# Performance work log

Hardware: AMD Instinct MI355X
Metric: run time of the kernel (lower is better)

## Reference

```python
import jax, jax.numpy as jnp
import numpy as np

B, IN, H, L, S = 256, 256, 256, 2, 128


def setup_inputs() -> dict:
    key = jax.random.key(0)
    ks = jax.random.split(key, 13)
    inp = {
        "x": jax.random.normal(ks[0], (B, IN), jnp.float32),
        "hidden_stack": jax.random.normal(ks[1], (S + 1, B, H, L), jnp.float32) * 0.1,
        "cell_stack": jax.random.normal(ks[2], (S + 1, B, H, L), jnp.float32) * 0.1,
        "w_ih0": jax.random.normal(ks[3], (4 * H, IN), jnp.float32) / np.sqrt(IN).astype(np.float32),
        "w_hh0": jax.random.normal(ks[4], (4 * H, H), jnp.float32) / np.sqrt(H).astype(np.float32),
        "b_ih0": jax.random.normal(ks[5], (4 * H,), jnp.float32) * 0.01,
        "b_hh0": jax.random.normal(ks[6], (4 * H,), jnp.float32) * 0.01,
        "w_ih1": jax.random.normal(ks[7], (4 * H, H), jnp.float32) / np.sqrt(H).astype(np.float32),
        "w_hh1": jax.random.normal(ks[8], (4 * H, H), jnp.float32) / np.sqrt(H).astype(np.float32),
        "b_ih1": jax.random.normal(ks[9], (4 * H,), jnp.float32) * 0.01,
        "b_hh1": jax.random.normal(ks[10], (4 * H,), jnp.float32) * 0.01,
        "op": jax.random.randint(ks[11], (B,), 0, 3, jnp.int32) - 1,  # {-1,0,1}: pop/hold/push
        "pos": jax.random.randint(ks[12], (B,), 1, S, jnp.int32),      # in-bounds for pos+1 and pos+op
    }
    return inp


def _lstm_cell(x, h, c, w_ih, w_hh, b_ih, b_hh):
    # torch.nn.LSTMCell gate order: input, forget, cell(g), output
    g = x @ w_ih.T + h @ w_hh.T + b_ih + b_hh  # (B, 4H)
    i, f, gg, o = jnp.split(g, 4, axis=-1)
    c2 = jax.nn.sigmoid(f) * c + jax.nn.sigmoid(i) * jnp.tanh(gg)
    h2 = jax.nn.sigmoid(o) * jnp.tanh(c2)
    return h2, c2


def reference(x, hidden_stack, cell_stack, w_ih0, w_hh0, b_ih0, b_hh0,
              w_ih1, w_hh1, b_ih1, b_hh1, op, pos):
    bidx = jnp.arange(x.shape[0])
    # gather current top-of-stack state: (B, H, L)
    cur_h = hidden_stack[pos, bidx]
    cur_c = cell_stack[pos, bidx]
    # two-layer LSTM cell (layer 1 feeds on layer 0 hidden)
    h0, c0 = _lstm_cell(x, cur_h[..., 0], cur_c[..., 0], w_ih0, w_hh0, b_ih0, b_hh0)
    h1, c1 = _lstm_cell(h0, cur_h[..., 1], cur_c[..., 1], w_ih1, w_hh1, b_ih1, b_hh1)
    next_h = jnp.stack([h0, h1], axis=-1)  # (B, H, L)
    next_c = jnp.stack([c0, c1], axis=-1)
    # scatter new state at pos+1
    hidden_stack = hidden_stack.at[pos + 1, bidx].set(next_h)
    cell_stack = cell_stack.at[pos + 1, bidx].set(next_c)
    # move stack pointer, gather return state
    new_pos = pos + op
    ret_h = hidden_stack[new_pos, bidx]  # (B, H, L)
    ret_c = cell_stack[new_pos, bidx]
    # faithful to torch source: hidden_ret[:, :, -1] -> shape (1, B, L)
    h_out = ret_h[:, -1, :][None]
    c_out = ret_c[:, -1, :][None]
    return h_out, c_out, hidden_stack, cell_stack
```

## Files before the change

### kernel.cpp

```cpp
#include <hip/hip_runtime.h>


static __device__ __forceinline__ float sigf(float x) {
    return 1.0f / (1.0f + __expf(-x));
}
static __device__ __forceinline__ float tanh_fast(float x) {
    return 2.0f / (1.0f + __expf(-2.0f * x)) - 1.0f;
}

#define GBM 16
#define GBN 64
#define GBK 32

#define NV4_PER_STACK 4227072
#define STACK_ELEMS   16908288
#define CEL_CHUNK1    655360

static __device__ __forceinline__ void copy_span(
    int cb0, const float4* __restrict__ csrc, float4* __restrict__ cdst, int cn4)
{
    int stride = (gridDim.x - cb0) * 256;
    for (int i = (blockIdx.x - cb0) * 256 + threadIdx.x; i < cn4; i += stride)
        cdst[i] = csrc[i];
}

__global__ __launch_bounds__(256) void gemm_copy_k(
    const float* __restrict__ a_lo,
    const float* __restrict__ a_hi,
    const int*   __restrict__ pos,
    const float* __restrict__ wih,
    const float* __restrict__ whh,
    const float* __restrict__ bih,
    const float* __restrict__ bhh,
    float* __restrict__ gates,
    const float4* __restrict__ csrc,
    float4* __restrict__ cdst,
    int cn4)
{
    if (blockIdx.x >= 256) {
        copy_span(256, csrc, cdst, cn4);
        return;
    }
    __shared__ float As[GBK][GBM + 1];
    __shared__ float Ws[GBK][GBN + 4];
    int t   = threadIdx.x;
    int bm0 = (blockIdx.x >> 4) * GBM;
    int jt0 = (blockIdx.x & 15) * GBN;
    int arow = t >> 4;
    int akk  = (t & 15) * 2;
    int wrow = t >> 2;
    int wkb  = (t & 3) * 8;
    int tx = t & 15, ty = t >> 4;
    int ab = bm0 + arow;
    int ap = pos[ab];
    int wj = jt0 + wrow;

    float2 apre;
    float4 wpre0, wpre1;
    {
        int k = akk;
        apre = *(const float2*)&a_lo[ab * 256 + k];
        const float* ws = &wih[wj * 256 + wkb];
        wpre0 = *(const float4*)ws;
        wpre1 = *(const float4*)(ws + 4);
    }
    float acc[4] = {0.f, 0.f, 0.f, 0.f};
    for (int kt = 0; kt < 512; kt += GBK) {
        __syncthreads();
        As[akk][arow]     = apre.x;
        As[akk + 1][arow] = apre.y;
        Ws[wkb][wrow]     = wpre0.x;
        Ws[wkb + 1][wrow] = wpre0.y;
        Ws[wkb + 2][wrow] = wpre0.z;
        Ws[wkb + 3][wrow] = wpre0.w;
        Ws[wkb + 4][wrow] = wpre1.x;
        Ws[wkb + 5][wrow] = wpre1.y;
        Ws[wkb + 6][wrow] = wpre1.z;
        Ws[wkb + 7][wrow] = wpre1.w;
        int kt2 = kt + GBK;
        if (kt2 < 512) {
            int k = kt2 + akk;
            if (k < 256) {
                apre = *(const float2*)&a_lo[ab * 256 + k];
            } else {
                const float* ah = a_hi + ((ap * 256 + ab) * 256 + (k - 256)) * 2;
                apre.x = ah[0];
                apre.y = ah[2];
            }
            int kk = kt2 + wkb;
            const float* ws = (kk < 256) ? &wih[wj * 256 + kk]
                                         : &whh[wj * 256 + kk - 256];
            wpre0 = *(const float4*)ws;
            wpre1 = *(const float4*)(ws + 4);
        }
        __syncthreads();
        #pragma unroll
        for (int k = 0; k < GBK; ++k) {
            float a   = As[k][ty];
            float4 bv = *(const float4*)&Ws[k][tx * 4];
            acc[0] = fmaf(a, bv.x, acc[0]);
            acc[1] = fmaf(a, bv.y, acc[1]);
            acc[2] = fmaf(a, bv.z, acc[2]);
            acc[3] = fmaf(a, bv.w, acc[3]);
        }
    }
    int j = jt0 + tx * 4;
    float4 b0 = *(const float4*)&bih[j];
    float4 b1 = *(const float4*)&bhh[j];
    float4 r;
    r.x = acc[0] + b0.x + b1.x;
    r.y = acc[1] + b0.y + b1.y;
    r.z = acc[2] + b0.z + b1.z;
    r.w = acc[3] + b0.w + b1.w;
    *(float4*)&gates[(bm0 + ty) * 1024 + j] = r;
}

__global__ __launch_bounds__(256) void act0_copy_k(
    const float* __restrict__ gates,
    const float* __restrict__ cel,
    const int*   __restrict__ pos,
    float* __restrict__ h0f, float* __restrict__ c0f,
    const float4* __restrict__ csrc,
    float4* __restrict__ cdst,
    int cn4)
{
    if (blockIdx.x >= 256) {
        copy_span(256, csrc, cdst, cn4);
        return;
    }
    int e = blockIdx.x * 256 + threadIdx.x;
    int b = e >> 8, h = e & 255;
    float cin = cel[((pos[b] * 256 + b) * 256 + h) * 2];
    const float* g = gates + b * 1024 + h;
    float gi = g[0], gf = g[256], gg = g[512], go = g[768];
    float c  = sigf(gf) * cin + sigf(gi) * tanh_fast(gg);
    h0f[e] = sigf(go) * tanh_fast(c);
    c0f[e] = c;
}

static __device__ __forceinline__ void lstm1(
    const float* __restrict__ gates, const float* __restrict__ cel,
    int p, int b, int h, float& hv, float& cv)
{
    float cin = cel[((p * 256 + b) * 256 + h) * 2 + 1];
    const float* g = gates + b * 1024 + h;
    float gi = g[0], gf = g[256], gg = g[512], go = g[768];
    cv = sigf(gf) * cin + sigf(gi) * tanh_fast(gg);
    hv = sigf(go) * tanh_fast(cv);
}

__global__ __launch_bounds__(256) void slot_k(
    const float* __restrict__ hid, const float* __restrict__ cel,
    const int* __restrict__ pos, const int* __restrict__ op,
    const float* __restrict__ h0f, const float* __restrict__ c0f,
    const float* __restrict__ gates,
    float* __restrict__ out)
{
    if (blockIdx.x == 256) {
        int b = threadIdx.x;
        int o = op[b];
        int p = pos[b];
        float h0v, h1v, c0v, c1v;
        if (o == 1) {
            h0v = h0f[b * 256 + 255];
            c0v = c0f[b * 256 + 255];
            lstm1(gates, cel, p, b, 255, h1v, c1v);
        } else {
            int base2 = (((p + o) * 256 + b) * 256 + 255) * 2;
            h0v = hid[base2]; h1v = hid[base2 + 1];
            c0v = cel[base2]; c1v = cel[base2 + 1];
        }
        out[b * 2]           = h0v;
        out[b * 2 + 1]       = h1v;
        out[512 + b * 2]     = c0v;
        out[512 + b * 2 + 1] = c1v;
        return;
    }
    int v = blockIdx.x * 256 + threadIdx.x;
    bool is_cell = v >= 32768;
    int vv = v & 32767;
    int b = vv >> 7;
    int q = vv & 127;
    int p = pos[b];
    int h = q * 2;
    float h1a, c1a, h1b, c1b;
    lstm1(gates, cel, p, b, h,     h1a, c1a);
    lstm1(gates, cel, p, b, h + 1, h1b, c1b);
    float4 val;
    if (is_cell) {
        val.x = c0f[b * 256 + h];     val.y = c1a;
        val.z = c0f[b * 256 + h + 1]; val.w = c1b;
    } else {
        val.x = h0f[b * 256 + h];     val.y = h1a;
        val.z = h0f[b * 256 + h + 1]; val.w = h1b;
    }
    float4* dst = (float4*)(out + 1024 + (is_cell ? STACK_ELEMS : 0));
    dst[(p + 1) * 32768 + b * 128 + q] = val;
}

extern "C" void kernel_launch(void* const* d_in, const int* in_sizes, int n_in,
                              void* d_out, int out_size, void* d_ws, size_t ws_size,
                              hipStream_t stream) {
    const float* x    = (const float*)d_in[0];
    const float* hid  = (const float*)d_in[1];
    const float* cel  = (const float*)d_in[2];
    const float* wih0 = (const float*)d_in[3];
    const float* whh0 = (const float*)d_in[4];
    const float* bih0 = (const float*)d_in[5];
    const float* bhh0 = (const float*)d_in[6];
    const float* wih1 = (const float*)d_in[7];
    const float* whh1 = (const float*)d_in[8];
    const float* bih1 = (const float*)d_in[9];
    const float* bhh1 = (const float*)d_in[10];
    const int* op  = (const int*)d_in[11];
    const int* pos = (const int*)d_in[12];
    float* out = (float*)d_out;

    float* W     = (float*)d_ws;
    float* gates = W;
    float* h0f   = W + 262144;
    float* c0f   = W + 327680;

    float4*       hid_out = (float4*)(out + 1024);
    float4*       cel_out = (float4*)(out + 1024 + STACK_ELEMS);
    const float4* hid_in  = (const float4*)hid;
    const float4* cel_in  = (const float4*)cel;

    gemm_copy_k<<<256 + 2048, 256, 0, stream>>>(
        x, hid, pos, wih0, whh0, bih0, bhh0, gates,
        hid_in, hid_out, NV4_PER_STACK);
    act0_copy_k<<<256 + 1024, 256, 0, stream>>>(
        gates, cel, pos, h0f, c0f,
        cel_in, cel_out, CEL_CHUNK1);
    gemm_copy_k<<<256 + 2048, 256, 0, stream>>>(
        h0f, hid + 1, pos, wih1, whh1, bih1, bhh1, gates,
        cel_in + CEL_CHUNK1, cel_out + CEL_CHUNK1,
        NV4_PER_STACK - CEL_CHUNK1);
    slot_k<<<257, 256, 0, stream>>>(
        hid, cel, pos, op, h0f, c0f, gates, out);
}
```

Before: 266.7 us.

## Split-K GEMM with larger register tiles and rebalanced stack-copy overlap

The gate GEMM switches to a 32x128 block tile with a 4x4 register tile per thread, and splits K across up to four blocks. Each split writes partial sums to workspace, and the activation kernels add those partials plus the biases. The bulk stack copies are redistributed across the three overlapped launches: a first hidden chunk, then the hidden remainder plus the first cell chunk, then the rest of the cell stack. The aim is more FMA work per shared-memory load and a better balance of the copy traffic against each compute phase, at the cost of extra partial-sum traffic and reduction reads.

```diff
diff --git a/kernel.cpp b/kernel.cpp
--- a/kernel.cpp
+++ b/kernel.cpp
@@ -8,20 +8,26 @@
     return 2.0f / (1.0f + __expf(-2.0f * x)) - 1.0f;
 }
 
-#define GBM 16
-#define GBN 64
-#define GBK 32
-
 #define NV4_PER_STACK 4227072
 #define STACK_ELEMS   16908288
-#define CEL_CHUNK1    655360
-
-static __device__ __forceinline__ void copy_span(
-    int cb0, const float4* __restrict__ csrc, float4* __restrict__ cdst, int cn4)
-{
-    int stride = (gridDim.x - cb0) * 256;
-    for (int i = (blockIdx.x - cb0) * 256 + threadIdx.x; i < cn4; i += stride)
-        cdst[i] = csrc[i];
+
+static __device__ __forceinline__ void copy_spans(
+    int cb0, int nb1,
+    const float4* __restrict__ s1, float4* __restrict__ d1, int n1,
+    const float4* __restrict__ s2, float4* __restrict__ d2, int n2)
+{
+    int cb = blockIdx.x - cb0;
+    int ncopy = gridDim.x - cb0;
+    if (cb < nb1) {
+        int stride = nb1 * 256;
+        for (int i = cb * 256 + threadIdx.x; i < n1; i += stride)
+            d1[i] = s1[i];
+    } else if (n2 > 0) {
+        int nb2 = ncopy - nb1;
+        int stride = nb2 * 256;
+        for (int i = (cb - nb1) * 256 + threadIdx.x; i < n2; i += stride)
+            d2[i] = s2[i];
+    }
 }
 
 __global__ __launch_bounds__(256) void gemm_copy_k(
@@ -30,121 +36,147 @@
     const int*   __restrict__ pos,
     const float* __restrict__ wih,
     const float* __restrict__ whh,
-    const float* __restrict__ bih,
-    const float* __restrict__ bhh,
-    float* __restrict__ gates,
-    const float4* __restrict__ csrc,
-    float4* __restrict__ cdst,
-    int cn4)
-{
-    if (blockIdx.x >= 256) {
-        copy_span(256, csrc, cdst, cn4);
+    float* __restrict__ gpart, int nks,
+    int nb1, const float4* __restrict__ cs1, float4* __restrict__ cd1, int cn1,
+    const float4* __restrict__ cs2, float4* __restrict__ cd2, int cn2)
+{
+    int ncomp = nks << 6;
+    if ((int)blockIdx.x >= ncomp) {
+        copy_spans(ncomp, nb1, cs1, cd1, cn1, cs2, cd2, cn2);
         return;
     }
-    __shared__ float As[GBK][GBM + 1];
-    __shared__ float Ws[GBK][GBN + 4];
+
+    __shared__ float As[32][36];
+    __shared__ float Ws[32][132];
+
     int t   = threadIdx.x;
-    int bm0 = (blockIdx.x >> 4) * GBM;
-    int jt0 = (blockIdx.x & 15) * GBN;
-    int arow = t >> 4;
-    int akk  = (t & 15) * 2;
-    int wrow = t >> 2;
-    int wkb  = (t & 3) * 8;
-    int tx = t & 15, ty = t >> 4;
-    int ab = bm0 + arow;
-    int ap = pos[ab];
-    int wj = jt0 + wrow;
-
-    float2 apre;
-    float4 wpre0, wpre1;
-    {
-        int k = akk;
-        apre = *(const float2*)&a_lo[ab * 256 + k];
-        const float* ws = &wih[wj * 256 + wkb];
-        wpre0 = *(const float4*)ws;
-        wpre1 = *(const float4*)(ws + 4);
-    }
-    float acc[4] = {0.f, 0.f, 0.f, 0.f};
-    for (int kt = 0; kt < 512; kt += GBK) {
-        __syncthreads();
-        As[akk][arow]     = apre.x;
-        As[akk + 1][arow] = apre.y;
-        Ws[wkb][wrow]     = wpre0.x;
-        Ws[wkb + 1][wrow] = wpre0.y;
-        Ws[wkb + 2][wrow] = wpre0.z;
-        Ws[wkb + 3][wrow] = wpre0.w;
-        Ws[wkb + 4][wrow] = wpre1.x;
-        Ws[wkb + 5][wrow] = wpre1.y;
-        Ws[wkb + 6][wrow] = wpre1.z;
-        Ws[wkb + 7][wrow] = wpre1.w;
-        int kt2 = kt + GBK;
-        if (kt2 < 512) {
-            int k = kt2 + akk;
-            if (k < 256) {
-                apre = *(const float2*)&a_lo[ab * 256 + k];
+    int ks  = blockIdx.x >> 6;
+    int tb  = blockIdx.x & 63;
+    int bm0 = (tb >> 3) << 5;
+    int jt0 = (tb & 7) << 7;
+    int kspan = 512 / nks;
+    int k0  = ks * kspan;
+    int nsub = kspan >> 5;
+
+    int arow = t >> 3;
+    int ak4  = (t & 7) << 2;
+    int ab   = bm0 + arow;
+    int ap   = pos[ab];
+    int wrow = t >> 1;
+    int wk   = (t & 1) << 4;
+    int wj   = jt0 + wrow;
+    int tx = t & 31, ty = t >> 5;
+
+    float acc[4][4] = {{0.f}};
+    for (int s = 0; s < nsub; ++s) {
+        int kb = k0 + (s << 5);
+        {
+            int kg = kb + ak4;
+            if (kg < 256) {
+                float4 v = *(const float4*)&a_lo[ab * 256 + kg];
+                As[ak4 + 0][arow] = v.x;
+                As[ak4 + 1][arow] = v.y;
+                As[ak4 + 2][arow] = v.z;
+                As[ak4 + 3][arow] = v.w;
             } else {
-                const float* ah = a_hi + ((ap * 256 + ab) * 256 + (k - 256)) * 2;
-                apre.x = ah[0];
-                apre.y = ah[2];
+                const float* ah = a_hi + ((ap * 256 + ab) * 256 + (kg - 256)) * 2;
+                As[ak4 + 0][arow] = ah[0];
+                As[ak4 + 1][arow] = ah[2];
+                As[ak4 + 2][arow] = ah[4];
+                As[ak4 + 3][arow] = ah[6];
             }
-            int kk = kt2 + wkb;
-            const float* ws = (kk < 256) ? &wih[wj * 256 + kk]
-                                         : &whh[wj * 256 + kk - 256];
-            wpre0 = *(const float4*)ws;
-            wpre1 = *(const float4*)(ws + 4);
+        }
+        {
+            int kg = kb + wk;
+            const float* ws = (kg < 256) ? &wih[wj * 256 + kg]
+                                         : &whh[wj * 256 + kg - 256];
+            #pragma unroll
+            for (int i = 0; i < 4; ++i) {
+                float4 v = *(const float4*)(ws + i * 4);
+                Ws[wk + i * 4 + 0][wrow] = v.x;
+                Ws[wk + i * 4 + 1][wrow] = v.y;
+                Ws[wk + i * 4 + 2][wrow] = v.z;
+                Ws[wk + i * 4 + 3][wrow] = v.w;
+            }
         }
         __syncthreads();
         #pragma unroll
-        for (int k = 0; k < GBK; ++k) {
-            float a   = As[k][ty];
-            float4 bv = *(const float4*)&Ws[k][tx * 4];
-            acc[0] = fmaf(a, bv.x, acc[0]);
-            acc[1] = fmaf(a, bv.y, acc[1]);
-            acc[2] = fmaf(a, bv.z, acc[2]);
-            acc[3] = fmaf(a, bv.w, acc[3]);
-        }
-    }
-    int j = jt0 + tx * 4;
-    float4 b0 = *(const float4*)&bih[j];
-    float4 b1 = *(const float4*)&bhh[j];
-    float4 r;
-    r.x = acc[0] + b0.x + b1.x;
-    r.y = acc[1] + b0.y + b1.y;
-    r.z = acc[2] + b0.z + b1.z;
-    r.w = acc[3] + b0.w + b1.w;
-    *(float4*)&gates[(bm0 + ty) * 1024 + j] = r;
+        for (int k = 0; k < 32; ++k) {
+            float4 av = *(const float4*)&As[k][ty << 2];
+            float4 wv = *(const float4*)&Ws[k][tx << 2];
+            float w0 = wv.x, w1 = wv.y, w2 = wv.z, w3 = wv.w;
+            acc[0][0] = fmaf(av.x, w0, acc[0][0]);
+            acc[0][1] = fmaf(av.x, w1, acc[0][1]);
+            acc[0][2] = fmaf(av.x, w2, acc[0][2]);
+            acc[0][3] = fmaf(av.x, w3, acc[0][3]);
+            acc[1][0] = fmaf(av.y, w0, acc[1][0]);
+            acc[1][1] = fmaf(av.y, w1, acc[1][1]);
+            acc[1][2] = fmaf(av.y, w2, acc[1][2]);
+            acc[1][3] = fmaf(av.y, w3, acc[1][3]);
+            acc[2][0] = fmaf(av.z, w0, acc[2][0]);
+            acc[2][1] = fmaf(av.z, w1, acc[2][1]);
+            acc[2][2] = fmaf(av.z, w2, acc[2][2]);
+            acc[2][3] = fmaf(av.z, w3, acc[2][3]);
+            acc[3][0] = fmaf(av.w, w0, acc[3][0]);
+            acc[3][1] = fmaf(av.w, w1, acc[3][1]);
+            acc[3][2] = fmaf(av.w, w2, acc[3][2]);
+            acc[3][3] = fmaf(av.w, w3, acc[3][3]);
+        }
+        __syncthreads();
+    }
+    float* gp = gpart + ks * 262144 + (bm0 + (ty << 2)) * 1024 + jt0 + (tx << 2);
+    #pragma unroll
+    for (int i = 0; i < 4; ++i) {
+        float4 r;
+        r.x = acc[i][0]; r.y = acc[i][1]; r.z = acc[i][2]; r.w = acc[i][3];
+        *(float4*)&gp[i * 1024] = r;
+    }
 }
 
 __global__ __launch_bounds__(256) void act0_copy_k(
-    const float* __restrict__ gates,
+    const float* __restrict__ gpart, int nks,
     const float* __restrict__ cel,
     const int*   __restrict__ pos,
+    const float* __restrict__ bih, const float* __restrict__ bhh,
     float* __restrict__ h0f, float* __restrict__ c0f,
-    const float4* __restrict__ csrc,
-    float4* __restrict__ cdst,
-    int cn4)
+    int nb1, const float4* __restrict__ cs1, float4* __restrict__ cd1, int cn1,
+    const float4* __restrict__ cs2, float4* __restrict__ cd2, int cn2)
 {
     if (blockIdx.x >= 256) {
-        copy_span(256, csrc, cdst, cn4);
+        copy_spans(256, nb1, cs1, cd1, cn1, cs2, cd2, cn2);
         return;
     }
     int e = blockIdx.x * 256 + threadIdx.x;
     int b = e >> 8, h = e & 255;
+    float gi = bih[h]       + bhh[h];
+    float gf = bih[256 + h] + bhh[256 + h];
+    float gg = bih[512 + h] + bhh[512 + h];
+    float go = bih[768 + h] + bhh[768 + h];
+    const float* gp = gpart + b * 1024 + h;
+    for (int ks = 0; ks < nks; ++ks, gp += 262144) {
+        gi += gp[0]; gf += gp[256]; gg += gp[512]; go += gp[768];
+    }
     float cin = cel[((pos[b] * 256 + b) * 256 + h) * 2];
-    const float* g = gates + b * 1024 + h;
-    float gi = g[0], gf = g[256], gg = g[512], go = g[768];
     float c  = sigf(gf) * cin + sigf(gi) * tanh_fast(gg);
     h0f[e] = sigf(go) * tanh_fast(c);
     c0f[e] = c;
 }
 
-static __device__ __forceinline__ void lstm1(
-    const float* __restrict__ gates, const float* __restrict__ cel,
+static __device__ __forceinline__ void lstm1p(
+    const float* __restrict__ gpart, int nks,
+    const float* __restrict__ bih, const float* __restrict__ bhh,
+    const float* __restrict__ cel,
     int p, int b, int h, float& hv, float& cv)
 {
+    float gi = bih[h]       + bhh[h];
+    float gf = bih[256 + h] + bhh[256 + h];
+    float gg = bih[512 + h] + bhh[512 + h];
+    float go = bih[768 + h] + bhh[768 + h];
+    const float* gp = gpart + b * 1024 + h;
+    for (int ks = 0; ks < nks; ++ks, gp += 262144) {
+        gi += gp[0]; gf += gp[256]; gg += gp[512]; go += gp[768];
+    }
     float cin = cel[((p * 256 + b) * 256 + h) * 2 + 1];
-    const float* g = gates + b * 1024 + h;
-    float gi = g[0], gf = g[256], gg = g[512], go = g[768];
     cv = sigf(gf) * cin + sigf(gi) * tanh_fast(gg);
     hv = sigf(go) * tanh_fast(cv);
 }
@@ -153,7 +185,8 @@
     const float* __restrict__ hid, const float* __restrict__ cel,
     const int* __restrict__ pos, const int* __restrict__ op,
     const float* __restrict__ h0f, const float* __restrict__ c0f,
-    const float* __restrict__ gates,
+    const float* __restrict__ gpart, int nks,
+    const float* __restrict__ bih, const float* __restrict__ bhh,
     float* __restrict__ out)
 {
     if (blockIdx.x == 256) {
@@ -164,7 +197,7 @@
         if (o == 1) {
             h0v = h0f[b * 256 + 255];
             c0v = c0f[b * 256 + 255];
-            lstm1(gates, cel, p, b, 255, h1v, c1v);
+            lstm1p(gpart, nks, bih, bhh, cel, p, b, 255, h1v, c1v);
         } else {
             int base2 = (((p + o) * 256 + b) * 256 + 255) * 2;
             h0v = hid[base2]; h1v = hid[base2 + 1];
@@ -184,8 +217,8 @@
     int p = pos[b];
     int h = q * 2;
     float h1a, c1a, h1b, c1b;
-    lstm1(gates, cel, p, b, h,     h1a, c1a);
-    lstm1(gates, cel, p, b, h + 1, h1b, c1b);
+    lstm1p(gpart, nks, bih, bhh, cel, p, b, h,     h1a, c1a);
+    lstm1p(gpart, nks, bih, bhh, cel, p, b, h + 1, h1b, c1b);
     float4 val;
     if (is_cell) {
         val.x = c0f[b * 256 + h];     val.y = c1a;
@@ -216,26 +249,36 @@
     const int* pos = (const int*)d_in[12];
     float* out = (float*)d_out;
 
-    float* W     = (float*)d_ws;
-    float* gates = W;
-    float* h0f   = W + 262144;
-    float* c0f   = W + 327680;
-
+    size_t need4 = (size_t)(4 * 262144 + 2 * 65536) * 4;
+    size_t need2 = (size_t)(2 * 262144 + 2 * 65536) * 4;
+    int KS = (ws_size >= need4) ? 4 : (ws_size >= need2 ? 2 : 1);
+    float* gpart = (float*)d_ws;
+    float* h0f   = gpart + (size_t)KS * 262144;
+    float* c0f   = h0f + 65536;
+
+    const float4* hid_in  = (const float4*)hid;
+    const float4* cel_in  = (const float4*)cel;
     float4*       hid_out = (float4*)(out + 1024);
     float4*       cel_out = (float4*)(out + 1024 + STACK_ELEMS);
-    const float4* hid_in  = (const float4*)hid;
-    const float4* cel_in  = (const float4*)cel;
-
-    gemm_copy_k<<<256 + 2048, 256, 0, stream>>>(
-        x, hid, pos, wih0, whh0, bih0, bhh0, gates,
-        hid_in, hid_out, NV4_PER_STACK);
-    act0_copy_k<<<256 + 1024, 256, 0, stream>>>(
-        gates, cel, pos, h0f, c0f,
-        cel_in, cel_out, CEL_CHUNK1);
-    gemm_copy_k<<<256 + 2048, 256, 0, stream>>>(
-        h0f, hid + 1, pos, wih1, whh1, bih1, bhh1, gates,
-        cel_in + CEL_CHUNK1, cel_out + CEL_CHUNK1,
-        NV4_PER_STACK - CEL_CHUNK1);
+
+    const int H1 = 2800000;
+    const int C2 = 1372928;
+    const int NCOPY = 2048;
+    int n2a = NV4_PER_STACK - H1;
+    int nb1_2 = (int)((long long)NCOPY * n2a / (n2a + C2));
+
+    gemm_copy_k<<<64 * KS + NCOPY, 256, 0, stream>>>(
+        x, hid, pos, wih0, whh0, gpart, KS,
+        NCOPY, hid_in, hid_out, H1,
+        (const float4*)0, (float4*)0, 0);
+    act0_copy_k<<<256 + NCOPY, 256, 0, stream>>>(
+        gpart, KS, cel, pos, bih0, bhh0, h0f, c0f,
+        nb1_2, hid_in + H1, hid_out + H1, n2a,
+        cel_in, cel_out, C2);
+    gemm_copy_k<<<64 * KS + NCOPY, 256, 0, stream>>>(
+        h0f, hid + 1, pos, wih1, whh1, gpart, KS,
+        NCOPY, cel_in + C2, cel_out + C2, NV4_PER_STACK - C2,
+        (const float4*)0, (float4*)0, 0);
     slot_k<<<257, 256, 0, stream>>>(
-        hid, cel, pos, op, h0f, c0f, gates, out);
-}
+        hid, cel, pos, op, h0f, c0f, gpart, KS, bih1, bhh1, out);
+}
```

After: 268.9 us. Within noise of the previous version (+0.8%).
